# Kernel optimization log

Measured on AMD Instinct MI355X. Metric: run time of the kernel, lower is better.

Reference implementation:

```python
import jax, jax.numpy as jnp
import numpy as np

B, S, D = 2, 2048, 1024
H, HD = 16, 64  # n_heads, head_dim


def setup_inputs() -> dict:
    key = jax.random.key(0)
    ks = jax.random.split(key, 6)
    scale = 1.0 / np.sqrt(D)
    return {
        "Q": jax.random.normal(ks[0], (B, S, D), dtype=jnp.float32),
        "K": jax.random.normal(ks[1], (B, S, D), dtype=jnp.float32),
        "V": jax.random.normal(ks[2], (B, S, D), dtype=jnp.float32),
        "Wq": jax.random.normal(ks[3], (H, D, HD), dtype=jnp.float32) * scale,
        "Wv": jax.random.normal(ks[4], (H, D, HD), dtype=jnp.float32) * scale,
        "Wo": jax.random.normal(ks[5], (D, D), dtype=jnp.float32) * scale,
        "bo": jnp.zeros((D,), dtype=jnp.float32),
    }


def reference(Q, K, V, Wq, Wv, Wo, bo):
    # NOTE: original code projects K with the *query* weight (bug kept for fidelity).
    q = jnp.einsum("bsd,hdk->bhsk", Q, Wq)   # [B,H,S,HD]
    k = jnp.einsum("bsd,hdk->bhsk", K, Wq)   # query weights, per original
    v = jnp.einsum("bsd,hdk->bhsk", V, Wv)
    scores = jnp.einsum("bhsk,bhtk->bhst", q, k) / jnp.sqrt(jnp.asarray(HD, q.dtype))
    weights = jax.nn.softmax(scores, axis=-1)  # [B,H,S,S]
    attn = jnp.einsum("bhst,bhtk->bhsk", weights, v)  # [B,H,S,HD]
    concat = attn.transpose(0, 2, 1, 3).reshape(Q.shape[0], Q.shape[1], H * HD)
    return concat @ Wo.T + bo
```

## Files before the change

kernel.cpp:

```cpp
#include <hip/hip_runtime.h>

typedef __attribute__((ext_vector_type(8))) short short8;
typedef __attribute__((ext_vector_type(4))) short short4v;
typedef __attribute__((ext_vector_type(4))) float f32x4;
typedef __attribute__((ext_vector_type(16))) float f32x16;

__device__ __forceinline__ unsigned short f2bf(float f) {
  union { float f; unsigned u; } v; v.f = f;
  unsigned u = v.u;
  unsigned r = (u + 0x7FFFu + ((u >> 16) & 1u)) >> 16;
  return (unsigned short)r;
}

__device__ __forceinline__ unsigned cvtpk(float lo, float hi) {
  unsigned r;
  asm("v_cvt_pk_bf16_f32 %0, %1, %2" : "=v"(r) : "v"(lo), "v"(hi));
  return r;
}

#if __has_builtin(__builtin_amdgcn_exp2f)
__device__ __forceinline__ float exp2_fast(float x) { return __builtin_amdgcn_exp2f(x); }
#else
__device__ __forceinline__ float exp2_fast(float x) { return __expf(x * 0.69314718056f); }
#endif

__device__ __forceinline__ void gl16(const void* g, void* l) {
  __builtin_amdgcn_global_load_lds(
      (const __attribute__((address_space(1))) unsigned int*)g,
      (__attribute__((address_space(3))) unsigned int*)l, 16, 0, 0);
}

#define QSCALE 0.1803368801111f

__global__ __launch_bounds__(256)
void pc_k(const float* __restrict__ Wq, const float* __restrict__ Wv,
          const float* __restrict__ Wo, const float* __restrict__ Q,
          const float* __restrict__ K, const float* __restrict__ V,
          unsigned short* __restrict__ BqT, unsigned short* __restrict__ BvT,
          unsigned short* __restrict__ BoT, unsigned short* __restrict__ QKVb) {
  __shared__ float tile[64 * 65];
  const int bidx = blockIdx.x;
  const int tid = threadIdx.x;
  if (bidx < 512) {
    const float* W = (bidx < 256) ? Wq : Wv;
    unsigned short* Bt = (bidx < 256) ? BqT : BvT;
    const int bb = bidx & 255;
    const int h  = bb >> 4;
    const int d0 = (bb & 15) * 64;
#pragma unroll
    for (int i = 0; i < 16; ++i) {
      int e = i * 256 + tid;
      int r = e >> 6, c = e & 63;
      tile[r * 65 + c] = W[(size_t)h * 65536 + (size_t)(d0 + r) * 64 + c];
    }
    __syncthreads();
#pragma unroll
    for (int i = 0; i < 16; ++i) {
      int e = i * 256 + tid;
      int jj = e >> 6, dd = e & 63;
      Bt[(size_t)(h * 64 + jj) * 1024 + d0 + dd] = f2bf(tile[dd * 65 + jj]);
    }
  } else if (bidx < 1536) {
    size_t t = (size_t)(bidx - 512) * 256 + tid;
    float4 f = *(const float4*)(Wo + t * 4);
    short4v v;
    v[0] = (short)f2bf(f.x); v[1] = (short)f2bf(f.y);
    v[2] = (short)f2bf(f.z); v[3] = (short)f2bf(f.w);
    *(short4v*)((short*)BoT + t * 4) = v;
  } else {
    const int cb = bidx - 1536;
    const int sec = cb >> 11;
    const float* src = (sec == 0) ? Q : (sec == 1) ? K : V;
    const float scale = (sec == 0) ? QSCALE : 1.0f;
    size_t t = (size_t)(cb & 2047) * 256 + tid;
    const float* s = src + t * 8;
    float4 f0 = *(const float4*)s;
    float4 f1 = *(const float4*)(s + 4);
    short8 v;
    v[0] = (short)f2bf(f0.x * scale); v[1] = (short)f2bf(f0.y * scale);
    v[2] = (short)f2bf(f0.z * scale); v[3] = (short)f2bf(f0.w * scale);
    v[4] = (short)f2bf(f1.x * scale); v[5] = (short)f2bf(f1.y * scale);
    v[6] = (short)f2bf(f1.z * scale); v[7] = (short)f2bf(f1.w * scale);
    *(short8*)(QKVb + (size_t)sec * 4194304 + t * 8) = v;
  }
}

template<int EPI>
__global__ __launch_bounds__(256, 2)
void gemm3_k(const unsigned short* __restrict__ A, const unsigned short* __restrict__ Bt,
             void* __restrict__ Cp, const float* __restrict__ bias) {
  __shared__ __attribute__((aligned(16))) unsigned short As[2][64 * 64];
  __shared__ __attribute__((aligned(16))) unsigned short Bs[2][128 * 64];
  const int tid = threadIdx.x;
  const int l = tid & 63;
  const int w = tid >> 6;
  const int wr = w >> 1, wc = w & 1;
  const int lg = l >> 4, lc = l & 15;
  const int nwg = (int)gridDim.x;
  const int bid = blockIdx.x;
  const int swz = (bid & 7) * (nwg >> 3) + (bid >> 3);
  const int bm = swz >> 3, bn = swz & 7;

  const int sr = tid >> 3, ss = tid & 7;
  const unsigned short* Asrc = A  + (size_t)(bm * 64  + sr) * 1024 + ((ss ^ (sr & 7)) * 8);
  const unsigned short* Bsrc = Bt + (size_t)(bn * 128 + sr) * 1024 + ((ss ^ (sr & 7)) * 8);

  f32x4 acc[2][4] = {};

  auto stage = [&](int bufn, int k0) {
    char* ad = (char*)&As[bufn][0] + tid * 16;
    char* bd = (char*)&Bs[bufn][0] + tid * 16;
    gl16(Asrc + k0,          ad);
    gl16(Asrc + 32768 + k0,  ad + 4096);
    gl16(Bsrc + k0,          bd);
    gl16(Bsrc + 32768 + k0,  bd + 4096);
    gl16(Bsrc + 65536 + k0,  bd + 8192);
    gl16(Bsrc + 98304 + k0,  bd + 12288);
  };

  stage(0, 0);
  __syncthreads();

  int buf = 0;
  for (int it = 0; it < 16; ++it) {
    if (it < 15) stage(buf ^ 1, (it + 1) * 64);
    const unsigned short* Ac = &As[buf][0];
    const unsigned short* Bc = &Bs[buf][0];
    short8 af[2][2], bf[4][2];
#pragma unroll
    for (int mi = 0; mi < 2; ++mi)
#pragma unroll
      for (int ks = 0; ks < 2; ++ks)
        af[mi][ks] = *(const short8*)&Ac[(wr * 32 + mi * 16 + lc) * 64 + (((ks * 4 + lg) ^ (lc & 7)) * 8)];
#pragma unroll
    for (int ni = 0; ni < 4; ++ni)
#pragma unroll
      for (int ks = 0; ks < 2; ++ks)
        bf[ni][ks] = *(const short8*)&Bc[(wc * 64 + ni * 16 + lc) * 64 + (((ks * 4 + lg) ^ (lc & 7)) * 8)];
#pragma unroll
    for (int mi = 0; mi < 2; ++mi)
#pragma unroll
      for (int ni = 0; ni < 4; ++ni) {
        acc[mi][ni] = __builtin_amdgcn_mfma_f32_16x16x32_bf16(af[mi][0], bf[ni][0], acc[mi][ni], 0, 0, 0);
        acc[mi][ni] = __builtin_amdgcn_mfma_f32_16x16x32_bf16(af[mi][1], bf[ni][1], acc[mi][ni], 0, 0, 0);
      }
    __syncthreads();
    buf ^= 1;
  }

  const int m0 = bm * 64 + wr * 32 + lg * 4;
  const int n0 = bn * 128 + wc * 64 + lc;
#pragma unroll
  for (int mi = 0; mi < 2; ++mi) {
#pragma unroll
    for (int ni = 0; ni < 4; ++ni) {
      if (EPI == 1) {
        int m = m0 + mi * 16;
        int bb = m >> 11, s = m & 2047;
        int n = n0 + ni * 16;
        int hh = n >> 6, hd = n & 63;
        short4v pk;
#pragma unroll
        for (int j = 0; j < 4; ++j) pk[j] = (short)f2bf(acc[mi][ni][j]);
        *(short4v*)((unsigned short*)Cp + (size_t)((bb * 16 + hh) * 64 + hd) * 2048 + s) = pk;
      } else {
#pragma unroll
        for (int j = 0; j < 4; ++j) {
          int m = m0 + mi * 16 + j;
          int n = n0 + ni * 16;
          if (EPI == 2) ((float*)Cp)[(size_t)m * 1024 + n] = acc[mi][ni][j] + bias[n];
          else          ((unsigned short*)Cp)[(size_t)m * 1024 + n] = f2bf(acc[mi][ni][j]);
        }
      }
    }
  }
}

__global__ __launch_bounds__(256, 2)
void gemm4_k(const unsigned short* __restrict__ A, const unsigned short* __restrict__ Bt,
             unsigned short* __restrict__ Cp) {
  __shared__ __attribute__((aligned(16))) unsigned short As[2][128 * 64];
  __shared__ __attribute__((aligned(16))) unsigned short Bs[2][128 * 64];
  const int tid = threadIdx.x;
  const int l = tid & 63;
  const int w = tid >> 6;
  const int wr = w >> 1, wc = w & 1;
  const int lg = l >> 4, lc = l & 15;
  const int nwg = (int)gridDim.x;
  const int bid = blockIdx.x;
  const int swz = (bid & 7) * (nwg >> 3) + (bid >> 3);
  const int bm = swz >> 3, bn = swz & 7;

  const int sr = tid >> 3, ss = tid & 7;
  const unsigned short* Asrc = A  + (size_t)(bm * 128 + sr) * 1024 + ((ss ^ (sr & 7)) * 8);
  const unsigned short* Bsrc = Bt + (size_t)(bn * 128 + sr) * 1024 + ((ss ^ (sr & 7)) * 8);

  f32x4 acc[4][4] = {};

  auto stage = [&](int bufn, int k0) {
    char* ad = (char*)&As[bufn][0] + tid * 16;
    char* bd = (char*)&Bs[bufn][0] + tid * 16;
#pragma unroll
    for (int p = 0; p < 4; ++p) {
      gl16(Asrc + (size_t)p * 32768 + k0, ad + p * 4096);
      gl16(Bsrc + (size_t)p * 32768 + k0, bd + p * 4096);
    }
  };

  stage(0, 0);
  __syncthreads();

  int buf = 0;
  for (int it = 0; it < 16; ++it) {
    if (it < 15) stage(buf ^ 1, (it + 1) * 64);
    const unsigned short* Ac = &As[buf][0];
    const unsigned short* Bc = &Bs[buf][0];
    short8 af[4][2], bf[4][2];
#pragma unroll
    for (int mi = 0; mi < 4; ++mi)
#pragma unroll
      for (int ks = 0; ks < 2; ++ks)
        af[mi][ks] = *(const short8*)&Ac[(wr * 64 + mi * 16 + lc) * 64 + (((ks * 4 + lg) ^ (lc & 7)) * 8)];
#pragma unroll
    for (int ni = 0; ni < 4; ++ni)
#pragma unroll
      for (int ks = 0; ks < 2; ++ks)
        bf[ni][ks] = *(const short8*)&Bc[(wc * 64 + ni * 16 + lc) * 64 + (((ks * 4 + lg) ^ (lc & 7)) * 8)];
#pragma unroll
    for (int mi = 0; mi < 4; ++mi)
#pragma unroll
      for (int ni = 0; ni < 4; ++ni) {
        acc[mi][ni] = __builtin_amdgcn_mfma_f32_16x16x32_bf16(af[mi][0], bf[ni][0], acc[mi][ni], 0, 0, 0);
        acc[mi][ni] = __builtin_amdgcn_mfma_f32_16x16x32_bf16(af[mi][1], bf[ni][1], acc[mi][ni], 0, 0, 0);
      }
    __syncthreads();
    buf ^= 1;
  }

  const int m0 = bm * 128 + wr * 64 + lg * 4;
  const int n0 = bn * 128 + wc * 64 + lc;
#pragma unroll
  for (int mi = 0; mi < 4; ++mi)
#pragma unroll
    for (int ni = 0; ni < 4; ++ni)
#pragma unroll
      for (int j = 0; j < 4; ++j)
        Cp[(size_t)(m0 + mi * 16 + j) * 1024 + n0 + ni * 16] = f2bf(acc[mi][ni][j]);
}

#define PACK8(SV, B0, W)                                                   \
  {                                                                        \
    float e0 = exp2_fast(SV[B0 + 0]), e1 = exp2_fast(SV[B0 + 1]);          \
    float e2 = exp2_fast(SV[B0 + 2]), e3 = exp2_fast(SV[B0 + 3]);          \
    float e4 = exp2_fast(SV[B0 + 4]), e5 = exp2_fast(SV[B0 + 5]);          \
    float e6 = exp2_fast(SV[B0 + 6]), e7 = exp2_fast(SV[B0 + 7]);          \
    l_r += ((e0 + e1) + (e2 + e3)) + ((e4 + e5) + (e6 + e7));              \
    unsigned Wa = cvtpk(e0, e1), Wb = cvtpk(e2, e3);                       \
    unsigned Wc = cvtpk(e4, e5), Wd = cvtpk(e6, e7);                       \
    unsigned pWa = __shfl_xor((int)Wa, 32), pWb = __shfl_xor((int)Wb, 32); \
    unsigned pWc = __shfl_xor((int)Wc, 32), pWd = __shfl_xor((int)Wd, 32); \
    W.x = hi ? pWc : Wa; W.y = hi ? pWd : Wb;                              \
    W.z = hi ? Wc : pWa; W.w = hi ? Wd : pWb;                              \
  }

__global__ __launch_bounds__(512, 4)
void attn_k(const unsigned short* __restrict__ qh, const unsigned short* __restrict__ kh,
            const unsigned short* __restrict__ vT, unsigned short* __restrict__ attnc) {
  __shared__ __attribute__((aligned(16))) short smem[32768];

  const int bid = (blockIdx.x & 7) * 64 + (blockIdx.x >> 3);
  const int qt = bid & 15;
  const int h = (bid >> 4) & 15;
  const int b = bid >> 8;
  const int tid = threadIdx.x;
  const int l = tid & 63;
  const int w = tid >> 6;
  const int g4 = w & 3;
  const int hf = w >> 2;
  const int q = l & 31;
  const int hi = l >> 5;
  const int ax = l & 7;

  const unsigned short* qb  = qh + (size_t)(b * 2048) * 1024 + h * 64;
  const unsigned short* kbf = kh + (size_t)(b * 2048) * 1024 + h * 64;
  const unsigned short* vb  = vT + (size_t)((b * 16 + h) * 64) * 2048;

  short* Kgrp = smem + hf * 16384;

  const int t = tid & 255;
  const int sr = t >> 3, ss = t & 7;
  const unsigned short* Ksrc = kbf + (size_t)(hf * 1024 + sr) * 1024 + ((ss ^ (sr & 7)) * 8);
  const unsigned short* Vsrc = vb + (size_t)sr * 2048 + hf * 1024 + ((ss ^ (sr & 7)) * 8);

  const int s0 = qt * 128 + g4 * 32;
  short8 qf[4];
#pragma unroll
  for (int c = 0; c < 4; ++c)
    qf[c] = *(const short8*)(qb + (size_t)(s0 + q) * 1024 + c * 16 + hi * 8);

  float l_r = 0.f;
  f32x16 acc0 = {}, acc1 = {};
  const f32x16 zero16 = {};

  auto stageKV = [&](int bufn, int i) {
    char* kd = (char*)(Kgrp + bufn * 4096) + t * 16;
    char* vd = (char*)(Kgrp + 8192 + bufn * 4096) + t * 16;
    const unsigned short* ks = Ksrc + (size_t)i * 65536;
    const unsigned short* vs = Vsrc + i * 64;
    gl16(ks,         kd);
    gl16(ks + 32768, kd + 4096);
    gl16(vs,         vd);
    gl16(vs + 65536, vd + 4096);
  };

  stageKV(0, 0);
  __syncthreads();

  int cur = 0;
  for (int i = 0; i < 16; ++i) {
    if (i < 15) stageKV(cur ^ 1, i + 1);

    const short* Kc = Kgrp + cur * 4096;
    f32x16 sv0 = zero16, sv1 = zero16;
#pragma unroll
    for (int c = 0; c < 4; ++c) {
      const int gofs = (((c * 2 + hi) ^ ax) * 8);
      short8 kf0 = *(const short8*)&Kc[(q) * 64 + gofs];
      short8 kf1 = *(const short8*)&Kc[(32 + q) * 64 + gofs];
      sv0 = __builtin_amdgcn_mfma_f32_32x32x16_bf16(kf0, qf[c], sv0, 0, 0, 0);
      sv1 = __builtin_amdgcn_mfma_f32_32x32x16_bf16(kf1, qf[c], sv1, 0, 0, 0);
    }

    uint4 w0, w1, w2, w3;
    PACK8(sv0, 0, w0);
    PACK8(sv0, 8, w1);
    PACK8(sv1, 0, w2);
    PACK8(sv1, 8, w3);
    short8 pf0 = *reinterpret_cast<short8*>(&w0);
    short8 pf1 = *reinterpret_cast<short8*>(&w1);
    short8 pf2 = *reinterpret_cast<short8*>(&w2);
    short8 pf3 = *reinterpret_cast<short8*>(&w3);

    const short* Vc = Kgrp + 8192 + cur * 4096;
#pragma unroll
    for (int kc = 0; kc < 4; ++kc) {
      const int gofs = (((kc * 2 + hi) ^ ax) * 8);
      short8 vf0 = *(const short8*)&Vc[(q) * 64 + gofs];
      short8 vf1 = *(const short8*)&Vc[(32 + q) * 64 + gofs];
      short8 pf = (kc == 0) ? pf0 : (kc == 1) ? pf1 : (kc == 2) ? pf2 : pf3;
      acc0 = __builtin_amdgcn_mfma_f32_32x32x16_bf16(vf0, pf, acc0, 0, 0, 0);
      acc1 = __builtin_amdgcn_mfma_f32_32x32x16_bf16(vf1, pf, acc1, 0, 0, 0);
    }

    __syncthreads();
    cur ^= 1;
  }

  l_r += __shfl_xor(l_r, 32);

  float* C = (float*)smem;
  if (hf == 1) {
    float* c = C + (size_t)(tid - 256) * 36;
    *(f32x4*)(c + 0)  = (f32x4){acc0[0], acc0[1], acc0[2], acc0[3]};
    *(f32x4*)(c + 4)  = (f32x4){acc0[4], acc0[5], acc0[6], acc0[7]};
    *(f32x4*)(c + 8)  = (f32x4){acc0[8], acc0[9], acc0[10], acc0[11]};
    *(f32x4*)(c + 12) = (f32x4){acc0[12], acc0[13], acc0[14], acc0[15]};
    *(f32x4*)(c + 16) = (f32x4){acc1[0], acc1[1], acc1[2], acc1[3]};
    *(f32x4*)(c + 20) = (f32x4){acc1[4], acc1[5], acc1[6], acc1[7]};
    *(f32x4*)(c + 24) = (f32x4){acc1[8], acc1[9], acc1[10], acc1[11]};
    *(f32x4*)(c + 28) = (f32x4){acc1[12], acc1[13], acc1[14], acc1[15]};
    c[32] = l_r;
  }
  __syncthreads();
  if (hf == 0) {
    const float* c = C + (size_t)tid * 36;
    float inv = 1.0f / (l_r + c[32]);

    unsigned short* outp = attnc + (size_t)(b * 2048 + s0 + q) * 1024 + h * 64;
#pragma unroll
    for (int t4 = 0; t4 < 4; ++t4) {
      short4v p0, p1;
#pragma unroll
      for (int n = 0; n < 4; ++n) {
        p0[n] = (short)f2bf((acc0[t4 * 4 + n] + c[t4 * 4 + n]) * inv);
        p1[n] = (short)f2bf((acc1[t4 * 4 + n] + c[16 + t4 * 4 + n]) * inv);
      }
      *(short4v*)(outp + (t4 * 8 + 4 * hi))      = p0;
      *(short4v*)(outp + (32 + t4 * 8 + 4 * hi)) = p1;
    }
  }
}

extern "C" void kernel_launch(void* const* d_in, const int* in_sizes, int n_in,
                              void* d_out, int out_size, void* d_ws, size_t ws_size,
                              hipStream_t stream) {
  const float* Q  = (const float*)d_in[0];
  const float* Kt = (const float*)d_in[1];
  const float* V  = (const float*)d_in[2];
  const float* Wq = (const float*)d_in[3];
  const float* Wv = (const float*)d_in[4];
  const float* Wo = (const float*)d_in[5];
  const float* bo = (const float*)d_in[6];
  float* out = (float*)d_out;

  char* ws = (char*)d_ws;
  unsigned short* QKb  = (unsigned short*)(ws);
  unsigned short* Vb   = (unsigned short*)(ws + ((size_t)16 << 20));
  unsigned short* qh   = (unsigned short*)(ws + ((size_t)24 << 20));
  unsigned short* BqT  = (unsigned short*)(ws + ((size_t)40 << 20));
  unsigned short* BvT  = (unsigned short*)(ws + ((size_t)42 << 20));
  unsigned short* BoT  = (unsigned short*)(ws + ((size_t)44 << 20));
  unsigned short* vT   = QKb;
  unsigned short* attc = (unsigned short*)(ws + ((size_t)8 << 20));
  unsigned short* kh   = qh + (size_t)4096 * 1024;

  pc_k<<<7680, 256, 0, stream>>>(Wq, Wv, Wo, Q, Kt, V, BqT, BvT, BoT, QKb);

  gemm4_k<<<512, 256, 0, stream>>>(QKb, BqT, qh);
  gemm3_k<1><<<512, 256, 0, stream>>>(Vb, BvT, vT, nullptr);

  attn_k<<<512, 512, 0, stream>>>(qh, kh, vT, attc);

  gemm3_k<2><<<512, 256, 0, stream>>>(attc, BoT, out, bo);
}
```

Baseline: 127.1 us.

## Merge Q/K and V projection GEMMs into one launch; raise MFMA priority in attention

Refactors the gemm4 kernel into a templated body and adds a combined kernel that runs the Q/K projection tiles and the V projection tiles (with the transposed-head epilogue) in a single 768-block grid. The workspace is re-laid out so vT no longer aliases the QK input buffer, which lets both GEMMs run concurrently. This saves a launch and the tail of one GEMM. The attention loop also wraps its MFMA sections in s_setprio to favour matrix issue across waves. A fallback keeps the old path when the workspace is too small.

```diff
diff --git a/kernel.cpp b/kernel.cpp
--- a/kernel.cpp
+++ b/kernel.cpp
@@ -176,20 +176,16 @@
   }
 }
 
-__global__ __launch_bounds__(256, 2)
-void gemm4_k(const unsigned short* __restrict__ A, const unsigned short* __restrict__ Bt,
-             unsigned short* __restrict__ Cp) {
-  __shared__ __attribute__((aligned(16))) unsigned short As[2][128 * 64];
-  __shared__ __attribute__((aligned(16))) unsigned short Bs[2][128 * 64];
+template<int EPI>
+__device__ __forceinline__
+void gemm4_body(unsigned short* AsB, unsigned short* BsB,
+                const unsigned short* __restrict__ A, const unsigned short* __restrict__ Bt,
+                unsigned short* __restrict__ Cp, int bm, int bn) {
   const int tid = threadIdx.x;
   const int l = tid & 63;
   const int w = tid >> 6;
   const int wr = w >> 1, wc = w & 1;
   const int lg = l >> 4, lc = l & 15;
-  const int nwg = (int)gridDim.x;
-  const int bid = blockIdx.x;
-  const int swz = (bid & 7) * (nwg >> 3) + (bid >> 3);
-  const int bm = swz >> 3, bn = swz & 7;
 
   const int sr = tid >> 3, ss = tid & 7;
   const unsigned short* Asrc = A  + (size_t)(bm * 128 + sr) * 1024 + ((ss ^ (sr & 7)) * 8);
@@ -198,8 +194,8 @@
   f32x4 acc[4][4] = {};
 
   auto stage = [&](int bufn, int k0) {
-    char* ad = (char*)&As[bufn][0] + tid * 16;
-    char* bd = (char*)&Bs[bufn][0] + tid * 16;
+    char* ad = (char*)AsB + bufn * 16384 + tid * 16;
+    char* bd = (char*)BsB + bufn * 16384 + tid * 16;
 #pragma unroll
     for (int p = 0; p < 4; ++p) {
       gl16(Asrc + (size_t)p * 32768 + k0, ad + p * 4096);
@@ -213,8 +209,8 @@
   int buf = 0;
   for (int it = 0; it < 16; ++it) {
     if (it < 15) stage(buf ^ 1, (it + 1) * 64);
-    const unsigned short* Ac = &As[buf][0];
-    const unsigned short* Bc = &Bs[buf][0];
+    const unsigned short* Ac = AsB + buf * 8192;
+    const unsigned short* Bc = BsB + buf * 8192;
     short8 af[4][2], bf[4][2];
 #pragma unroll
     for (int mi = 0; mi < 4; ++mi)
@@ -240,12 +236,52 @@
   const int m0 = bm * 128 + wr * 64 + lg * 4;
   const int n0 = bn * 128 + wc * 64 + lc;
 #pragma unroll
-  for (int mi = 0; mi < 4; ++mi)
-#pragma unroll
-    for (int ni = 0; ni < 4; ++ni)
-#pragma unroll
-      for (int j = 0; j < 4; ++j)
-        Cp[(size_t)(m0 + mi * 16 + j) * 1024 + n0 + ni * 16] = f2bf(acc[mi][ni][j]);
+  for (int mi = 0; mi < 4; ++mi) {
+#pragma unroll
+    for (int ni = 0; ni < 4; ++ni) {
+      if (EPI == 1) {
+        int m = m0 + mi * 16;
+        int bb = m >> 11, s = m & 2047;
+        int n = n0 + ni * 16;
+        int hh = n >> 6, hd = n & 63;
+        short4v pk;
+#pragma unroll
+        for (int j = 0; j < 4; ++j) pk[j] = (short)f2bf(acc[mi][ni][j]);
+        *(short4v*)(Cp + (size_t)((bb * 16 + hh) * 64 + hd) * 2048 + s) = pk;
+      } else {
+#pragma unroll
+        for (int j = 0; j < 4; ++j)
+          Cp[(size_t)(m0 + mi * 16 + j) * 1024 + n0 + ni * 16] = f2bf(acc[mi][ni][j]);
+      }
+    }
+  }
+}
+
+__global__ __launch_bounds__(256, 2)
+void gemm4_k(const unsigned short* __restrict__ A, const unsigned short* __restrict__ Bt,
+             unsigned short* __restrict__ Cp) {
+  __shared__ __attribute__((aligned(16))) unsigned short As[2 * 128 * 64];
+  __shared__ __attribute__((aligned(16))) unsigned short Bs[2 * 128 * 64];
+  const int nwg = (int)gridDim.x;
+  const int bid = blockIdx.x;
+  const int swz = (bid & 7) * (nwg >> 3) + (bid >> 3);
+  gemm4_body<0>(As, Bs, A, Bt, Cp, swz >> 3, swz & 7);
+}
+
+__global__ __launch_bounds__(256, 2)
+void gemm4qkv_k(const unsigned short* __restrict__ QKb, const unsigned short* __restrict__ Vb,
+                const unsigned short* __restrict__ BqT, const unsigned short* __restrict__ BvT,
+                unsigned short* __restrict__ qh, unsigned short* __restrict__ vT) {
+  __shared__ __attribute__((aligned(16))) unsigned short As[2 * 128 * 64];
+  __shared__ __attribute__((aligned(16))) unsigned short Bs[2 * 128 * 64];
+  const int bid = blockIdx.x;
+  const int swz = (bid & 7) * 96 + (bid >> 3);
+  if (swz < 512) {
+    gemm4_body<0>(As, Bs, QKb, BqT, qh, swz >> 3, swz & 7);
+  } else {
+    const int sv = swz - 512;
+    gemm4_body<1>(As, Bs, Vb, BvT, vT, sv >> 3, sv & 7);
+  }
 }
 
 #define PACK8(SV, B0, W)                                                   \
@@ -322,6 +358,7 @@
 
     const short* Kc = Kgrp + cur * 4096;
     f32x16 sv0 = zero16, sv1 = zero16;
+    __builtin_amdgcn_s_setprio(1);
 #pragma unroll
     for (int c = 0; c < 4; ++c) {
       const int gofs = (((c * 2 + hi) ^ ax) * 8);
@@ -330,6 +367,7 @@
       sv0 = __builtin_amdgcn_mfma_f32_32x32x16_bf16(kf0, qf[c], sv0, 0, 0, 0);
       sv1 = __builtin_amdgcn_mfma_f32_32x32x16_bf16(kf1, qf[c], sv1, 0, 0, 0);
     }
+    __builtin_amdgcn_s_setprio(0);
 
     uint4 w0, w1, w2, w3;
     PACK8(sv0, 0, w0);
@@ -342,6 +380,7 @@
     short8 pf3 = *reinterpret_cast<short8*>(&w3);
 
     const short* Vc = Kgrp + 8192 + cur * 4096;
+    __builtin_amdgcn_s_setprio(1);
 #pragma unroll
     for (int kc = 0; kc < 4; ++kc) {
       const int gofs = (((kc * 2 + hi) ^ ax) * 8);
@@ -351,6 +390,7 @@
       acc0 = __builtin_amdgcn_mfma_f32_32x32x16_bf16(vf0, pf, acc0, 0, 0, 0);
       acc1 = __builtin_amdgcn_mfma_f32_32x32x16_bf16(vf1, pf, acc1, 0, 0, 0);
     }
+    __builtin_amdgcn_s_setprio(0);
 
     __syncthreads();
     cur ^= 1;
@@ -402,24 +442,38 @@
   const float* Wo = (const float*)d_in[5];
   const float* bo = (const float*)d_in[6];
   float* out = (float*)d_out;
-
   char* ws = (char*)d_ws;
-  unsigned short* QKb  = (unsigned short*)(ws);
-  unsigned short* Vb   = (unsigned short*)(ws + ((size_t)16 << 20));
-  unsigned short* qh   = (unsigned short*)(ws + ((size_t)24 << 20));
-  unsigned short* BqT  = (unsigned short*)(ws + ((size_t)40 << 20));
-  unsigned short* BvT  = (unsigned short*)(ws + ((size_t)42 << 20));
-  unsigned short* BoT  = (unsigned short*)(ws + ((size_t)44 << 20));
-  unsigned short* vT   = QKb;
-  unsigned short* attc = (unsigned short*)(ws + ((size_t)8 << 20));
-  unsigned short* kh   = qh + (size_t)4096 * 1024;
-
-  pc_k<<<7680, 256, 0, stream>>>(Wq, Wv, Wo, Q, Kt, V, BqT, BvT, BoT, QKb);
-
-  gemm4_k<<<512, 256, 0, stream>>>(QKb, BqT, qh);
-  gemm3_k<1><<<512, 256, 0, stream>>>(Vb, BvT, vT, nullptr);
-
-  attn_k<<<512, 512, 0, stream>>>(qh, kh, vT, attc);
-
-  gemm3_k<2><<<512, 256, 0, stream>>>(attc, BoT, out, bo);
-}
+
+  if (ws_size >= ((size_t)54 << 20)) {
+    unsigned short* QKb  = (unsigned short*)(ws);
+    unsigned short* Vb   = (unsigned short*)(ws + ((size_t)16 << 20));
+    unsigned short* attc = Vb;
+    unsigned short* qh   = (unsigned short*)(ws + ((size_t)24 << 20));
+    unsigned short* kh   = qh + (size_t)4096 * 1024;
+    unsigned short* vT   = (unsigned short*)(ws + ((size_t)40 << 20));
+    unsigned short* BqT  = (unsigned short*)(ws + ((size_t)48 << 20));
+    unsigned short* BvT  = (unsigned short*)(ws + ((size_t)50 << 20));
+    unsigned short* BoT  = (unsigned short*)(ws + ((size_t)52 << 20));
+
+    pc_k<<<7680, 256, 0, stream>>>(Wq, Wv, Wo, Q, Kt, V, BqT, BvT, BoT, QKb);
+    gemm4qkv_k<<<768, 256, 0, stream>>>(QKb, Vb, BqT, BvT, qh, vT);
+    attn_k<<<512, 512, 0, stream>>>(qh, kh, vT, attc);
+    gemm3_k<2><<<512, 256, 0, stream>>>(attc, BoT, out, bo);
+  } else {
+    unsigned short* QKb  = (unsigned short*)(ws);
+    unsigned short* Vb   = (unsigned short*)(ws + ((size_t)16 << 20));
+    unsigned short* qh   = (unsigned short*)(ws + ((size_t)24 << 20));
+    unsigned short* BqT  = (unsigned short*)(ws + ((size_t)40 << 20));
+    unsigned short* BvT  = (unsigned short*)(ws + ((size_t)42 << 20));
+    unsigned short* BoT  = (unsigned short*)(ws + ((size_t)44 << 20));
+    unsigned short* vT   = QKb;
+    unsigned short* attc = (unsigned short*)(ws + ((size_t)8 << 20));
+    unsigned short* kh   = qh + (size_t)4096 * 1024;
+
+    pc_k<<<7680, 256, 0, stream>>>(Wq, Wv, Wo, Q, Kt, V, BqT, BvT, BoT, QKb);
+    gemm4_k<<<512, 256, 0, stream>>>(QKb, BqT, qh);
+    gemm3_k<1><<<512, 256, 0, stream>>>(Vb, BvT, vT, nullptr);
+    attn_k<<<512, 512, 0, stream>>>(qh, kh, vT, attc);
+    gemm3_k<2><<<512, 256, 0, stream>>>(attc, BoT, out, bo);
+  }
+}
```

Measured after the change: 127.8 us. No clear change (+0.6%).
